# Performance work log

Hardware: AMD Instinct MI355X
Metric: run time of the kernel (lower is better)

The kernel has to match this reference:

```python
import jax, jax.numpy as jnp
import numpy as np

B, T, N = 1, 1024, 8
D_S, D_R, H, TOPK = 1024, 512, 8, 4
DH_S, DH_R = D_S // H, D_R // H
EPS = 1e-6


def _rmsnorm(x, w):
    return x * jax.lax.rsqrt(jnp.mean(x * x, axis=-1, keepdims=True) + EPS) * w


def setup_inputs() -> dict:
    key = jax.random.key(0)
    ks = jax.random.split(key, 12)

    def lin(k, fan_in, fan_out):
        b = 1.0 / np.sqrt(fan_in)
        return jax.random.uniform(k, (fan_in, fan_out), jnp.float32, -b, b)

    return {
        "s": jax.random.normal(ks[0], (B, T, D_S), jnp.float32),
        "r": jax.random.normal(ks[1], (B, T, N, D_R), jnp.float32),
        "gate_v": jax.random.uniform(ks[2], (B, T, 1), dtype=jnp.float32),
        "norm_s_w": jnp.ones((D_S,), jnp.float32),
        "norm_r_w": jnp.ones((D_R,), jnp.float32),
        "Wsq": lin(ks[3], D_S, D_S),
        "Wsk": lin(ks[4], D_R, D_S),
        "Wsv": lin(ks[5], D_R, D_S),
        "Wso": lin(ks[6], D_S, D_S),
        "Wrq": lin(ks[7], D_R, D_R),
        "Wrk": lin(ks[8], D_S, D_R),
        "Wrv": lin(ks[9], D_S, D_R),
        "Wro": lin(ks[10], D_R, D_R),
    }


def reference(s, r, gate_v, norm_s_w, norm_r_w, Wsq, Wsk, Wsv, Wso, Wrq, Wrk, Wrv, Wro):
    scale_s = DH_S ** -0.5
    scale_r = DH_R ** -0.5
    s_n = _rmsnorm(s, norm_s_w)  # (B,T,D_S)
    r_n = _rmsnorm(r, norm_r_w)  # (B,T,N,D_R)

    # --- s reads its own prefix-local reasoning slots (_s_reads_prefix_r) ---
    q = (s_n @ Wsq).reshape(B, T, H, DH_S)
    k = (r_n @ Wsk).reshape(B, T, N, H, DH_S)
    v = (r_n @ Wsv).reshape(B, T, N, H, DH_S)
    w = jax.nn.softmax(jnp.einsum('bthd,btnhd->bthn', q, k) * scale_s, axis=-1)
    s2 = s + jnp.einsum('bthn,btnhd->bthd', w, v).reshape(B, T, D_S) @ Wso

    # --- reasoning slots attend causally over surface prefix (_r_reads_s_causal) ---
    qr = (r_n @ Wrq).reshape(B, T, N, H, DH_R)
    kr = (s_n @ Wrk).reshape(B, T, H, DH_R)
    vr = (s_n @ Wrv).reshape(B, T, H, DH_R)
    scores = jnp.einsum('btnhd,bphd->btnhp', qr, kr) * scale_r  # (B,T,N,H,T)
    causal = jnp.arange(T)[:, None] >= jnp.arange(T)[None, :]  # p <= t
    scores = jnp.where(causal[None, :, None, None, :], scores, -jnp.inf)
    wr = jax.nn.softmax(scores, axis=-1)
    r2 = r + jnp.einsum('btnhp,bphd->btnhd', wr, vr).reshape(B, T, N, D_R) @ Wro

    # --- sparse top-k prefix write-back (_sparse_prefix_r_to_s) ---
    qs = s_n @ Wsq                       # (B,T,D_S)
    ksp = r_n @ Wsk                      # (B,T,N,D_S)
    vsp = r_n @ Wsv                      # (B,T,N,D_S)
    sp = jnp.einsum('btd,btnd->btn', qs, ksp) * scale_s
    vals, idx = jax.lax.top_k(sp, TOPK)
    wk = jax.nn.softmax(vals, axis=-1)   # softmax over scattered -inf == softmax over top-k
    onehot = jax.nn.one_hot(idx, N, dtype=sp.dtype)  # (B,T,K,N)
    weights = jnp.einsum('btk,btkn->btn', wk, onehot)
    r_sparse = jnp.einsum('btn,btnd->btd', weights, vsp)

    return (s2 + gate_v * r_sparse, r2)
```

## Files before the change

kernel.cpp:

```cpp
#include <hip/hip_runtime.h>
#include <hip/hip_bf16.h>
#include <math.h>
#include <type_traits>


#define T_DIM 1024
#define N_SLOT 8
#define DS 1024
#define DR 512
#define NH 8
#define DHS 128
#define DHR 64

typedef __attribute__((ext_vector_type(8))) short short8v;
typedef __attribute__((ext_vector_type(4))) float floatx4;

#define GLDS(gptr, lptr)                                                     \
  __builtin_amdgcn_global_load_lds(                                          \
      (__attribute__((address_space(1))) void*)(gptr),                       \
      (__attribute__((address_space(3))) void*)(lptr), 16, 0, 0)

__device__ inline int xcd_swz(int b, int G) {
  int per = G >> 3, rem = G & 7;
  int x = b & 7, i = b >> 3;
  return x * per + (x < rem ? x : rem) + i;
}

__device__ inline float bf_lo(unsigned int u) {
  unsigned short x = (unsigned short)(u & 0xffff);
  __hip_bfloat16 b;
  __builtin_memcpy(&b, &x, 2);
  return __bfloat162float(b);
}
__device__ inline float bf_hi(unsigned int u) {
  unsigned short x = (unsigned short)(u >> 16);
  __hip_bfloat16 b;
  __builtin_memcpy(&b, &x, 2);
  return __bfloat162float(b);
}

struct TJob { const float* W; __hip_bfloat16* Wt; int K; int N; float scale; int b0; };
struct TJobs { TJob j[8]; };

__global__ __launch_bounds__(256) void prep_kernel(
    TJobs jobs, const float* __restrict__ s, const float* __restrict__ r,
    const float* __restrict__ nsw, const float* __restrict__ nrw,
    __hip_bfloat16* __restrict__ s_nb, float* __restrict__ s_n32,
    __hip_bfloat16* __restrict__ r_nb) {
  __shared__ float sh[32][33];
  const int tid = threadIdx.x;
  if (blockIdx.x < 4608) {
    int ji = 0;
#pragma unroll
    for (int t = 1; t < 8; ++t)
      if ((int)blockIdx.x >= jobs.j[t].b0) ji = t;
    const TJob J = jobs.j[ji];
    const int lb = blockIdx.x - J.b0;
    const int nbx = J.N >> 5;
    const int n0 = (lb % nbx) * 32, k0 = (lb / nbx) * 32;
    const int tx = tid & 31, ty = tid >> 5;
#pragma unroll
    for (int i = 0; i < 4; ++i) {
      int kk = ty + i * 8;
      sh[kk][tx] = J.W[(size_t)(k0 + kk) * J.N + n0 + tx];
    }
    __syncthreads();
#pragma unroll
    for (int i = 0; i < 4; ++i) {
      int nn = ty + i * 8;
      J.Wt[(size_t)(n0 + nn) * J.K + k0 + tx] = __float2bfloat16(sh[tx][nn] * J.scale);
    }
  } else {
    const int blk = blockIdx.x - 4608;
    const bool is_s = blk < 1024;
    const int row = is_s ? blk : blk - 1024;
    const int width = is_s ? DS : DR;
    const float* x = is_s ? s : r;
    const float* w = is_s ? nsw : nrw;
    const size_t base = (size_t)row * width;
    float ss = 0.f;
    for (int i = tid; i < width; i += 256) {
      float v = x[base + i];
      ss += v * v;
    }
    for (int m = 32; m >= 1; m >>= 1) ss += __shfl_xor(ss, m);
    const int wave = tid >> 6, lane = tid & 63;
    if (lane == 0) sh[0][wave] = ss;
    __syncthreads();
    float total = sh[0][0] + sh[0][1] + sh[0][2] + sh[0][3];
    float scale = rsqrtf(total / (float)width + 1e-6f);
    for (int i = tid; i < width; i += 256) {
      float val = x[base + i] * scale * w[i];
      if (is_s) {
        s_nb[base + i] = __float2bfloat16(val);
        s_n32[base + i] = val;
      } else {
        r_nb[base + i] = __float2bfloat16(val);
      }
    }
  }
}

template <int BS, int TT, bool BT, bool BSUM>
__global__ __launch_bounds__(256) void gemm_f32_kernel(
    const float* __restrict__ A, const float* __restrict__ B,
    float* __restrict__ C, int M, int N, int K) {
  __shared__ __align__(16) float Ast[16][BS + 4];
  __shared__ __align__(16) float Bs[16][BS + 4];
  const int tid = threadIdx.x;
  const int tx = tid & 15, ty = tid >> 4;
  const int row0 = blockIdx.y * BS, col0 = blockIdx.x * BS;
  const int kz = blockIdx.z;
  const int kbeg = kz * (K >> 1), kend = kbeg + (K >> 1);
  float* Cz = C + (size_t)kz * M * N;
  const size_t bsz = (size_t)K * N;
  float acc[TT][TT] = {};
  constexpr int NF4 = BS * 16 / 4;
  for (int k0 = kbeg; k0 < kend; k0 += 16) {
    __syncthreads();
    for (int l = tid; l < NF4; l += 256) {
      int lr = l >> 2, lk = (l & 3) << 2;
      float4 a4 = *(const float4*)&A[(size_t)(row0 + lr) * K + k0 + lk];
      Ast[lk + 0][lr] = a4.x;
      Ast[lk + 1][lr] = a4.y;
      Ast[lk + 2][lr] = a4.z;
      Ast[lk + 3][lr] = a4.w;
      if (BT) {
        float4 b4 = *(const float4*)&B[(size_t)(col0 + lr) * K + k0 + lk];
        Bs[lk + 0][lr] = b4.x;
        Bs[lk + 1][lr] = b4.y;
        Bs[lk + 2][lr] = b4.z;
        Bs[lk + 3][lr] = b4.w;
      } else {
        int bkk = l / (BS / 4), bc = (l % (BS / 4)) << 2;
        size_t bidx = (size_t)(k0 + bkk) * N + col0 + bc;
        float4 b4 = *(const float4*)&B[bidx];
        if (BSUM) {
          float4 b2 = *(const float4*)&B[bsz + bidx];
          b4.x += b2.x; b4.y += b2.y; b4.z += b2.z; b4.w += b2.w;
        }
        *(float4*)&Bs[bkk][bc] = b4;
      }
    }
    __syncthreads();
#pragma unroll
    for (int kk = 0; kk < 16; ++kk) {
      float av[TT], bv[TT];
#pragma unroll
      for (int u = 0; u < TT; u += 4) {
        *(float4*)&av[u] = *(const float4*)&Ast[kk][ty * TT + u];
        *(float4*)&bv[u] = *(const float4*)&Bs[kk][tx * TT + u];
      }
#pragma unroll
      for (int i = 0; i < TT; ++i)
#pragma unroll
        for (int j = 0; j < TT; ++j) acc[i][j] += av[i] * bv[j];
    }
  }
#pragma unroll
  for (int i = 0; i < TT; ++i) {
    size_t crow = (size_t)(row0 + ty * TT + i) * N + col0;
#pragma unroll
    for (int j = 0; j < TT; j += 4) {
      *(float4*)&Cz[crow + tx * TT + j] =
          make_float4(acc[i][j], acc[i][j + 1], acc[i][j + 2], acc[i][j + 3]);
    }
  }
}

template <int MT, bool ACCUM, typename OutT, bool RADD = false>
__global__ __launch_bounds__(256) void mfma_gemm_kernel(
    const __hip_bfloat16* __restrict__ A, const __hip_bfloat16* __restrict__ Bt,
    OutT* __restrict__ C, const float* __restrict__ R, int M, int N, int K,
    int nbx) {
  constexpr int FR = MT / 32;
  constexpr int HALF = MT / 2;
  constexpr int SEG_PER_WAVE = MT / 16 / 4;
  __shared__ __hip_bfloat16 As[MT][32];
  __shared__ __hip_bfloat16 Bs[MT][32];
  const int sb = xcd_swz(blockIdx.x, gridDim.x);
  const int row0 = (sb / nbx) * MT, col0 = (sb % nbx) * MT;
  const int tid = threadIdx.x;
  const int lane = tid & 63, wave = tid >> 6;
  const int wm = wave >> 1, wn = wave & 1;
  const int l15 = lane & 15, l4 = lane >> 4;
  const int dma_r = lane >> 2;
  const int dma_c = (lane & 3) ^ ((lane >> 3) & 3);
  const int rd_sw = (l15 >> 1) & 3;
  floatx4 acc[FR][FR] = {};
  for (int k0 = 0; k0 < K; k0 += 32) {
    __syncthreads();
#pragma unroll
    for (int i = 0; i < SEG_PER_WAVE; ++i) {
      int seg = wave * SEG_PER_WAVE + i;
      GLDS(&A[(size_t)(row0 + seg * 16 + dma_r) * K + k0 + dma_c * 8], &As[seg * 16][0]);
      GLDS(&Bt[(size_t)(col0 + seg * 16 + dma_r) * K + k0 + dma_c * 8], &Bs[seg * 16][0]);
    }
    __syncthreads();
    short8v af[FR], bf[FR];
#pragma unroll
    for (int i = 0; i < FR; ++i)
      af[i] = *(const short8v*)&As[wm * HALF + i * 16 + l15][(l4 ^ rd_sw) * 8];
#pragma unroll
    for (int j = 0; j < FR; ++j)
      bf[j] = *(const short8v*)&Bs[wn * HALF + j * 16 + l15][(l4 ^ rd_sw) * 8];
#pragma unroll
    for (int i = 0; i < FR; ++i)
#pragma unroll
      for (int j = 0; j < FR; ++j)
        acc[i][j] = __builtin_amdgcn_mfma_f32_16x16x32_bf16(af[i], bf[j], acc[i][j], 0, 0, 0);
  }
#pragma unroll
  for (int i = 0; i < FR; ++i) {
    int rb = row0 + wm * HALF + i * 16 + l4 * 4;
#pragma unroll
    for (int j = 0; j < FR; ++j) {
      int cb = col0 + wn * HALF + j * 16 + l15;
#pragma unroll
      for (int rg = 0; rg < 4; ++rg) {
        size_t idx = (size_t)(rb + rg) * N + cb;
        if constexpr (std::is_same<OutT, __hip_bfloat16>::value) {
          C[idx] = __float2bfloat16(acc[i][j][rg]);
        } else if constexpr (RADD) {
          C[idx] = R[idx] + acc[i][j][rg];
        } else if constexpr (ACCUM) {
          C[idx] += acc[i][j][rg];
        } else {
          C[idx] = acc[i][j][rg];
        }
      }
    }
  }
}

struct GJob { const __hip_bfloat16* Bt; __hip_bfloat16* C; int N; int b0; int trans; };
struct GJobs { GJob j[3]; };

template <int MT>
__global__ __launch_bounds__(256) void mfma_gemm_batch_kernel(
    const __hip_bfloat16* __restrict__ A, GJobs jobs, int M, int K) {
  constexpr int FR = MT / 32;
  constexpr int HALF = MT / 2;
  constexpr int SEG_PER_WAVE = MT / 16 / 4;
  __shared__ __hip_bfloat16 As[MT][32];
  __shared__ __hip_bfloat16 Bs[MT][32];
  const int sb = xcd_swz(blockIdx.x, gridDim.x);
  int ji = 0;
#pragma unroll
  for (int t = 1; t < 3; ++t)
    if (sb >= jobs.j[t].b0) ji = t;
  const GJob J = jobs.j[ji];
  const int lb = sb - J.b0;
  const int nbx = J.N / MT;
  const int row0 = (lb / nbx) * MT, col0 = (lb % nbx) * MT;
  const int tid = threadIdx.x;
  const int lane = tid & 63, wave = tid >> 6;
  const int wm = wave >> 1, wn = wave & 1;
  const int l15 = lane & 15, l4 = lane >> 4;
  const int dma_r = lane >> 2;
  const int dma_c = (lane & 3) ^ ((lane >> 3) & 3);
  const int rd_sw = (l15 >> 1) & 3;
  floatx4 acc[FR][FR] = {};
  for (int k0 = 0; k0 < K; k0 += 32) {
    __syncthreads();
#pragma unroll
    for (int i = 0; i < SEG_PER_WAVE; ++i) {
      int seg = wave * SEG_PER_WAVE + i;
      GLDS(&A[(size_t)(row0 + seg * 16 + dma_r) * K + k0 + dma_c * 8], &As[seg * 16][0]);
      GLDS(&J.Bt[(size_t)(col0 + seg * 16 + dma_r) * K + k0 + dma_c * 8], &Bs[seg * 16][0]);
    }
    __syncthreads();
    short8v af[FR], bf[FR];
#pragma unroll
    for (int i = 0; i < FR; ++i)
      af[i] = *(const short8v*)&As[wm * HALF + i * 16 + l15][(l4 ^ rd_sw) * 8];
#pragma unroll
    for (int j = 0; j < FR; ++j)
      bf[j] = *(const short8v*)&Bs[wn * HALF + j * 16 + l15][(l4 ^ rd_sw) * 8];
#pragma unroll
    for (int i = 0; i < FR; ++i)
#pragma unroll
      for (int j = 0; j < FR; ++j)
        acc[i][j] = __builtin_amdgcn_mfma_f32_16x16x32_bf16(af[i], bf[j], acc[i][j], 0, 0, 0);
  }
#pragma unroll
  for (int i = 0; i < FR; ++i) {
    int rb = row0 + wm * HALF + i * 16 + l4 * 4;
#pragma unroll
    for (int j = 0; j < FR; ++j) {
      int cb = col0 + wn * HALF + j * 16 + l15;
      if (J.trans) {
        __hip_bfloat16 pk[4];
#pragma unroll
        for (int rg = 0; rg < 4; ++rg) pk[rg] = __float2bfloat16(acc[i][j][rg]);
        *(ushort4*)&J.C[(size_t)cb * M + rb] = *(const ushort4*)pk;
      } else {
#pragma unroll
        for (int rg = 0; rg < 4; ++rg)
          J.C[(size_t)(rb + rg) * J.N + cb] = __float2bfloat16(acc[i][j][rg]);
      }
    }
  }
}

__global__ __launch_bounds__(256) void part1_kernel(
    const float* __restrict__ s, const float* __restrict__ gv,
    const __hip_bfloat16* __restrict__ q, const __hip_bfloat16* __restrict__ k,
    const __hip_bfloat16* __restrict__ v, const float* __restrict__ r,
    const float* __restrict__ nrw, const float* __restrict__ u0,
    const float* __restrict__ u1, __hip_bfloat16* __restrict__ attn1,
    float* __restrict__ outS) {
  __shared__ float qs[DS];
  __shared__ float dots[NH][N_SLOT];
  __shared__ float wattn[NH][N_SLOT];
  __shared__ float w8[N_SLOT];
  __shared__ float spv[N_SLOT];
  __shared__ float gateL;
  const int t = blockIdx.x;
  const int tid = threadIdx.x;
  {
    const unsigned int* q2 = (const unsigned int*)&q[(size_t)t * DS];
    for (int i = tid; i < DS / 2; i += 256) {
      unsigned int pk = q2[i];
      qs[2 * i] = bf_lo(pk);
      qs[2 * i + 1] = bf_hi(pk);
    }
  }
  __syncthreads();
  const int wave = tid >> 6, lane = tid & 63;
#pragma unroll
  for (int e = 0; e < 16; ++e) {
    int pair = wave * 16 + e;
    int h = pair >> 3, n = pair & 7;
    const unsigned int* kr2 =
        (const unsigned int*)&k[((size_t)t * N_SLOT + n) * DS + h * DHS];
    unsigned int pk = kr2[lane];
    float a = qs[h * DHS + 2 * lane] * bf_lo(pk) +
              qs[h * DHS + 2 * lane + 1] * bf_hi(pk);
    for (int m = 32; m >= 1; m >>= 1) a += __shfl_xor(a, m);
    if (lane == 0) dots[h][n] = a;
  }
  const float scale_s = 0.08838834764831845f;
#pragma unroll
  for (int e = 0; e < 2; ++e) {
    const int n = wave * 2 + e;
    const float* rr = &r[((size_t)t * N_SLOT + n) * DR];
    const float* ub0 = &u0[(size_t)t * DR];
    const float* ub1 = &u1[(size_t)t * DR];
    float ssum = 0.f, dot = 0.f;
#pragma unroll
    for (int jj = 0; jj < 8; ++jj) {
      int j = lane + 64 * jj;
      float rv = rr[j];
      ssum += rv * rv;
      dot += rv * nrw[j] * (ub0[j] + ub1[j]);
    }
    for (int m = 32; m >= 1; m >>= 1) {
      ssum += __shfl_xor(ssum, m);
      dot += __shfl_xor(dot, m);
    }
    if (lane == 0) {
      float rs = rsqrtf(ssum / (float)DR + 1e-6f);
      spv[n] = scale_s * rs * dot;
    }
  }
  __syncthreads();
  if (tid < 8) {
    int h = tid;
    float vmax = -1e30f;
    for (int n = 0; n < 8; ++n) vmax = fmaxf(vmax, dots[h][n] * scale_s);
    float sum = 0.f;
    for (int n = 0; n < 8; ++n) {
      float e = __expf(dots[h][n] * scale_s - vmax);
      wattn[h][n] = e;
      sum += e;
    }
    float inv = 1.f / sum;
    for (int n = 0; n < 8; ++n) wattn[h][n] *= inv;
  }
  if (tid == 64) {
    float sv[8];
    for (int n = 0; n < 8; ++n) sv[n] = spv[n];
    bool used[8] = {};
    float vals[4];
    int idxs[4];
    for (int kk = 0; kk < 4; ++kk) {
      float best = -1e30f;
      int bi = 0;
      for (int n = 0; n < 8; ++n)
        if (!used[n] && sv[n] > best) { best = sv[n]; bi = n; }
      used[bi] = true;
      vals[kk] = best;
      idxs[kk] = bi;
    }
    float mx = vals[0];
    float wv[4];
    float sum = 0.f;
    for (int kk = 0; kk < 4; ++kk) {
      wv[kk] = __expf(vals[kk] - mx);
      sum += wv[kk];
    }
    float inv = 1.f / sum;
    for (int n = 0; n < 8; ++n) w8[n] = 0.f;
    for (int kk = 0; kk < 4; ++kk) w8[idxs[kk]] = wv[kk] * inv;
    gateL = gv[t];
  }
  __syncthreads();
  const float gate = gateL;
#pragma unroll
  for (int jj = 0; jj < 2; ++jj) {
    int dp = tid + 256 * jj;
    int hh = dp >> 6;
    float a1x = 0.f, a1y = 0.f, a2x = 0.f, a2y = 0.f;
#pragma unroll
    for (int n = 0; n < 8; ++n) {
      unsigned int pv =
          ((const unsigned int*)&v[((size_t)t * N_SLOT + n) * DS])[dp];
      float vx = bf_lo(pv), vy = bf_hi(pv);
      float wa = wattn[hh][n], wb = w8[n];
      a1x += wa * vx; a1y += wa * vy;
      a2x += wb * vx; a2y += wb * vy;
    }
    __hip_bfloat16 pk2[2] = {__float2bfloat16(a1x), __float2bfloat16(a1y)};
    ((unsigned int*)&attn1[(size_t)t * DS])[dp] = *(const unsigned int*)pk2;
    float2 sv = ((const float2*)&s[(size_t)t * DS])[dp];
    ((float2*)&outS[(size_t)t * DS])[dp] =
        make_float2(sv.x + gate * a2x, sv.y + gate * a2y);
  }
}

__global__ __launch_bounds__(256) void flash_mfma_kernel(
    const __hip_bfloat16* __restrict__ qb, const __hip_bfloat16* __restrict__ kb,
    const __hip_bfloat16* __restrict__ vbT, __hip_bfloat16* __restrict__ rat) {
  __shared__ __align__(16) __hip_bfloat16 QP[64][72];
  __shared__ __align__(16) __hip_bfloat16 Ks[64][72];
  __shared__ __align__(16) __hip_bfloat16 Vt[64][72];
  const int tid = threadIdx.x;
  const int lane = tid & 63, wave = tid >> 6;
  const int l15 = lane & 15, l4 = lane >> 4;
  const int h = blockIdx.y;
  const int qbase = blockIdx.x * 64;
  const int s = wave * 16;

  for (int g = tid; g < 512; g += 256) {
    int rr = g >> 3, c = (g & 7) * 8;
    *(ulonglong2*)&QP[rr][c] =
        *(const ulonglong2*)&qb[(size_t)(qbase + rr) * DR + h * DHR + c];
  }
  __syncthreads();
  short8v qf[2];
#pragma unroll
  for (int kk = 0; kk < 2; ++kk)
    qf[kk] = *(const short8v*)&QP[s + l15][kk * 32 + l4 * 8];

  const int myt = (qbase + s + l15) >> 3;
  const int tmin = (qbase + s) >> 3;
  const int tmax = (qbase + s + 15) >> 3;

  float m_r = -1e30f, l_r = 0.f;
  floatx4 o[4] = {};

  const int ntiles = (((qbase + 63) >> 3) >> 6) + 1;
  for (int pt = 0; pt < ntiles; ++pt) {
    const int p0 = pt << 6;
    __syncthreads();
    for (int g = tid; g < 512; g += 256) {
      int rr = g >> 3, c = (g & 7) * 8;
      *(ulonglong2*)&Ks[rr][c] =
          *(const ulonglong2*)&kb[(size_t)(p0 + rr) * DR + h * DHR + c];
      *(ulonglong2*)&Vt[rr][c] =
          *(const ulonglong2*)&vbT[(size_t)(h * DHR + rr) * T_DIM + p0 + c];
    }
    __syncthreads();
    if (p0 > tmax) continue;
    floatx4 sc[4] = {};
#pragma unroll
    for (int j = 0; j < 4; ++j)
#pragma unroll
      for (int kk = 0; kk < 2; ++kk) {
        short8v kf = *(const short8v*)&Ks[j * 16 + l15][kk * 32 + l4 * 8];
        sc[j] = __builtin_amdgcn_mfma_f32_16x16x32_bf16(kf, qf[kk], sc[j], 0, 0, 0);
      }
    if (p0 + 63 > tmin) {
#pragma unroll
      for (int j = 0; j < 4; ++j)
#pragma unroll
        for (int rg = 0; rg < 4; ++rg)
          if (p0 + j * 16 + l4 * 4 + rg > myt) sc[j][rg] = -1e30f;
    }
    float mx = m_r;
#pragma unroll
    for (int j = 0; j < 4; ++j)
#pragma unroll
      for (int rg = 0; rg < 4; ++rg) mx = fmaxf(mx, sc[j][rg]);
    mx = fmaxf(mx, __shfl_xor(mx, 16));
    mx = fmaxf(mx, __shfl_xor(mx, 32));
    float sum = 0.f;
#pragma unroll
    for (int j = 0; j < 4; ++j)
#pragma unroll
      for (int rg = 0; rg < 4; ++rg) {
        float e = __expf(sc[j][rg] - mx);
        sc[j][rg] = e;
        sum += e;
      }
    sum += __shfl_xor(sum, 16);
    sum += __shfl_xor(sum, 32);
    const float alpha = __expf(m_r - mx);
    l_r = alpha * l_r + sum;
    m_r = mx;
#pragma unroll
    for (int j = 0; j < 4; ++j) {
      __hip_bfloat16 pk[4];
#pragma unroll
      for (int rg = 0; rg < 4; ++rg) pk[rg] = __float2bfloat16(sc[j][rg]);
      *(ushort4*)&QP[s + l15][j * 16 + l4 * 4] = *(const ushort4*)pk;
    }
#pragma unroll
    for (int jd = 0; jd < 4; ++jd) o[jd] *= alpha;
#pragma unroll
    for (int kk = 0; kk < 2; ++kk) {
      short8v pf = *(const short8v*)&QP[s + l15][kk * 32 + l4 * 8];
#pragma unroll
      for (int jd = 0; jd < 4; ++jd) {
        short8v vf = *(const short8v*)&Vt[jd * 16 + l15][kk * 32 + l4 * 8];
        o[jd] = __builtin_amdgcn_mfma_f32_16x16x32_bf16(vf, pf, o[jd], 0, 0, 0);
      }
    }
  }
  const float inv = 1.f / l_r;
  const size_t rbase = (size_t)(qbase + s + l15) * DR + h * DHR;
#pragma unroll
  for (int jd = 0; jd < 4; ++jd) {
    __hip_bfloat16 pk[4];
#pragma unroll
    for (int rg = 0; rg < 4; ++rg) pk[rg] = __float2bfloat16(o[jd][rg] * inv);
    *(ushort4*)&rat[rbase + jd * 16 + l4 * 4] = *(const ushort4*)pk;
  }
}

extern "C" void kernel_launch(void* const* d_in, const int* in_sizes, int n_in,
                              void* d_out, int out_size, void* d_ws,
                              size_t ws_size, hipStream_t stream) {
  const float* s   = (const float*)d_in[0];
  const float* r   = (const float*)d_in[1];
  const float* gv  = (const float*)d_in[2];
  const float* nsw = (const float*)d_in[3];
  const float* nrw = (const float*)d_in[4];
  const float* Wsq = (const float*)d_in[5];
  const float* Wsk = (const float*)d_in[6];
  const float* Wsv = (const float*)d_in[7];
  const float* Wso = (const float*)d_in[8];
  const float* Wrq = (const float*)d_in[9];
  const float* Wrk = (const float*)d_in[10];
  const float* Wrv = (const float*)d_in[11];
  const float* Wro = (const float*)d_in[12];

  float* outS = (float*)d_out;
  float* outR = outS + 1048576;

  char* wp = (char*)d_ws;
  float* qreg = (float*)wp;           wp += 1048576 * 4;
  __hip_bfloat16* k   = (__hip_bfloat16*)wp; wp += 8388608 * 2;
  __hip_bfloat16* v   = (__hip_bfloat16*)wp; wp += 8388608 * 2;
  __hip_bfloat16* qrb = (__hip_bfloat16*)wp; wp += 4194304 * 2;
  __hip_bfloat16* krb = (__hip_bfloat16*)wp; wp += 524288 * 2;
  __hip_bfloat16* vrbT = (__hip_bfloat16*)wp; wp += 524288 * 2;
  __hip_bfloat16* s_nb = (__hip_bfloat16*)wp; wp += 1048576 * 2;
  __hip_bfloat16* r_nb = (__hip_bfloat16*)wp; wp += 4194304 * 2;
  __hip_bfloat16* WsqT = (__hip_bfloat16*)wp; wp += 1048576 * 2;
  __hip_bfloat16* WskT = (__hip_bfloat16*)wp; wp += 524288 * 2;
  __hip_bfloat16* WsvT = (__hip_bfloat16*)wp; wp += 524288 * 2;
  __hip_bfloat16* WsoT = (__hip_bfloat16*)wp; wp += 1048576 * 2;
  __hip_bfloat16* WrqT = (__hip_bfloat16*)wp; wp += 262144 * 2;
  __hip_bfloat16* WrkT = (__hip_bfloat16*)wp; wp += 524288 * 2;
  __hip_bfloat16* WrvT = (__hip_bfloat16*)wp; wp += 524288 * 2;
  __hip_bfloat16* WroT = (__hip_bfloat16*)wp; wp += 262144 * 2;

  float* s_n32 = qreg;
  __hip_bfloat16* q = (__hip_bfloat16*)qreg;
  float* Wc01 = (float*)r_nb;
  float* u0   = (float*)((char*)r_nb + 4194304);
  float* u1   = (float*)((char*)r_nb + 6291456);
  __hip_bfloat16* attn1b = s_nb;
  __hip_bfloat16* ratb   = r_nb;

  TJobs jobs = {{
      {Wsq, WsqT, 1024, 1024, 1.f, 0},
      {Wsk, WskT, 512, 1024, 1.f, 1024},
      {Wsv, WsvT, 512, 1024, 1.f, 1536},
      {Wso, WsoT, 1024, 1024, 1.f, 2048},
      {Wrq, WrqT, 512, 512, 0.125f, 3072},
      {Wrk, WrkT, 1024, 512, 1.f, 3328},
      {Wrv, WrvT, 1024, 512, 1.f, 3840},
      {Wro, WroT, 512, 512, 1.f, 4352},
  }};
  prep_kernel<<<13824, 256, 0, stream>>>(jobs, s, r, nsw, nrw, s_nb, s_n32, r_nb);

  GJobs ga = {{
      {WskT, k, 1024, 0, 0},
      {WsvT, v, 1024, 512, 0},
      {WrqT, qrb, 512, 1024, 0},
  }};
  mfma_gemm_batch_kernel<128><<<1280, 256, 0, stream>>>(r_nb, ga, 8192, 512);

  gemm_f32_kernel<64, 4, true, false><<<dim3(8, 16, 2), 256, 0, stream>>>(Wsq, Wsk, Wc01, 1024, 512, 1024);

  gemm_f32_kernel<64, 4, false, true><<<dim3(8, 16, 2), 256, 0, stream>>>(s_n32, Wc01, u0, 1024, 512, 1024);

  GJobs gb = {{
      {WsqT, q, 1024, 0, 0},
      {WrkT, krb, 512, 256, 0},
      {WrvT, vrbT, 512, 384, 1},
  }};
  mfma_gemm_batch_kernel<64><<<512, 256, 0, stream>>>(s_nb, gb, 1024, 1024);

  part1_kernel<<<1024, 256, 0, stream>>>(s, gv, q, k, v, r, nrw, u0, u1, attn1b, outS);

  mfma_gemm_kernel<64, true, float><<<256, 256, 0, stream>>>(attn1b, WsoT, outS, nullptr, 1024, 1024, 1024, 16);

  flash_mfma_kernel<<<dim3(128, 8), 256, 0, stream>>>(qrb, krb, vrbT, ratb);

  mfma_gemm_kernel<128, false, float, true><<<256, 256, 0, stream>>>(ratb, WroT, outR, r, 8192, 512, 512, 4);
}
```

Baseline: 318.9 us.

## Merge kernel launches into horizontally fused prep, GEMM, attention and epilogue kernels

Collapses the nine launches into four. The fp32 weight-combine GEMM is folded into the prep kernel. The fp32 u-GEMM and all six bf16 projection GEMMs run in one 128-tile merged kernel. The causal flash attention and the part1 per-token attention share one launch, and the two output projections share one epilogue kernel. Flash attention also gains register double-buffering of K/V tiles, and its query tiles are issued longest-first. Aliased workspace buffers are split into separate regions so the fused stages no longer overwrite each other's inputs. The aim is to cut launch gaps and tail underutilisation, at the cost of larger heterogeneous kernels whose register and shared-memory use is sized for the worst branch.

```diff
diff --git a/kernel.cpp b/kernel.cpp
--- a/kernel.cpp
+++ b/kernel.cpp
@@ -39,80 +39,18 @@
   return __bfloat162float(b);
 }
 
-struct TJob { const float* W; __hip_bfloat16* Wt; int K; int N; float scale; int b0; };
-struct TJobs { TJob j[8]; };
-
-__global__ __launch_bounds__(256) void prep_kernel(
-    TJobs jobs, const float* __restrict__ s, const float* __restrict__ r,
-    const float* __restrict__ nsw, const float* __restrict__ nrw,
-    __hip_bfloat16* __restrict__ s_nb, float* __restrict__ s_n32,
-    __hip_bfloat16* __restrict__ r_nb) {
-  __shared__ float sh[32][33];
-  const int tid = threadIdx.x;
-  if (blockIdx.x < 4608) {
-    int ji = 0;
-#pragma unroll
-    for (int t = 1; t < 8; ++t)
-      if ((int)blockIdx.x >= jobs.j[t].b0) ji = t;
-    const TJob J = jobs.j[ji];
-    const int lb = blockIdx.x - J.b0;
-    const int nbx = J.N >> 5;
-    const int n0 = (lb % nbx) * 32, k0 = (lb / nbx) * 32;
-    const int tx = tid & 31, ty = tid >> 5;
-#pragma unroll
-    for (int i = 0; i < 4; ++i) {
-      int kk = ty + i * 8;
-      sh[kk][tx] = J.W[(size_t)(k0 + kk) * J.N + n0 + tx];
-    }
-    __syncthreads();
-#pragma unroll
-    for (int i = 0; i < 4; ++i) {
-      int nn = ty + i * 8;
-      J.Wt[(size_t)(n0 + nn) * J.K + k0 + tx] = __float2bfloat16(sh[tx][nn] * J.scale);
-    }
-  } else {
-    const int blk = blockIdx.x - 4608;
-    const bool is_s = blk < 1024;
-    const int row = is_s ? blk : blk - 1024;
-    const int width = is_s ? DS : DR;
-    const float* x = is_s ? s : r;
-    const float* w = is_s ? nsw : nrw;
-    const size_t base = (size_t)row * width;
-    float ss = 0.f;
-    for (int i = tid; i < width; i += 256) {
-      float v = x[base + i];
-      ss += v * v;
-    }
-    for (int m = 32; m >= 1; m >>= 1) ss += __shfl_xor(ss, m);
-    const int wave = tid >> 6, lane = tid & 63;
-    if (lane == 0) sh[0][wave] = ss;
-    __syncthreads();
-    float total = sh[0][0] + sh[0][1] + sh[0][2] + sh[0][3];
-    float scale = rsqrtf(total / (float)width + 1e-6f);
-    for (int i = tid; i < width; i += 256) {
-      float val = x[base + i] * scale * w[i];
-      if (is_s) {
-        s_nb[base + i] = __float2bfloat16(val);
-        s_n32[base + i] = val;
-      } else {
-        r_nb[base + i] = __float2bfloat16(val);
-      }
-    }
-  }
-}
-
-template <int BS, int TT, bool BT, bool BSUM>
-__global__ __launch_bounds__(256) void gemm_f32_kernel(
-    const float* __restrict__ A, const float* __restrict__ B,
-    float* __restrict__ C, int M, int N, int K) {
-  __shared__ __align__(16) float Ast[16][BS + 4];
-  __shared__ __align__(16) float Bs[16][BS + 4];
+template <bool BT, bool BSUM>
+__device__ void gemm_f32_body(char* smemraw, const float* __restrict__ A,
+                              const float* __restrict__ B, float* __restrict__ C,
+                              int M, int N, int K, int bx, int by, int bz) {
+  constexpr int BS = 64, TT = 4;
+  float(*Ast)[BS + 4] = (float(*)[BS + 4])smemraw;
+  float(*Bs)[BS + 4] = (float(*)[BS + 4])(smemraw + 16 * (BS + 4) * 4);
   const int tid = threadIdx.x;
   const int tx = tid & 15, ty = tid >> 4;
-  const int row0 = blockIdx.y * BS, col0 = blockIdx.x * BS;
-  const int kz = blockIdx.z;
-  const int kbeg = kz * (K >> 1), kend = kbeg + (K >> 1);
-  float* Cz = C + (size_t)kz * M * N;
+  const int row0 = by * BS, col0 = bx * BS;
+  const int kbeg = bz * (K >> 1), kend = kbeg + (K >> 1);
+  float* Cz = C + (size_t)bz * M * N;
   const size_t bsz = (size_t)K * N;
   float acc[TT][TT] = {};
   constexpr int NF4 = BS * 16 / 4;
@@ -146,11 +84,8 @@
 #pragma unroll
     for (int kk = 0; kk < 16; ++kk) {
       float av[TT], bv[TT];
-#pragma unroll
-      for (int u = 0; u < TT; u += 4) {
-        *(float4*)&av[u] = *(const float4*)&Ast[kk][ty * TT + u];
-        *(float4*)&bv[u] = *(const float4*)&Bs[kk][tx * TT + u];
-      }
+      *(float4*)&av[0] = *(const float4*)&Ast[kk][ty * TT];
+      *(float4*)&bv[0] = *(const float4*)&Bs[kk][tx * TT];
 #pragma unroll
       for (int i = 0; i < TT; ++i)
 #pragma unroll
@@ -168,18 +103,104 @@
   }
 }
 
-template <int MT, bool ACCUM, typename OutT, bool RADD = false>
-__global__ __launch_bounds__(256) void mfma_gemm_kernel(
-    const __hip_bfloat16* __restrict__ A, const __hip_bfloat16* __restrict__ Bt,
-    OutT* __restrict__ C, const float* __restrict__ R, int M, int N, int K,
-    int nbx) {
-  constexpr int FR = MT / 32;
-  constexpr int HALF = MT / 2;
-  constexpr int SEG_PER_WAVE = MT / 16 / 4;
-  __shared__ __hip_bfloat16 As[MT][32];
-  __shared__ __hip_bfloat16 Bs[MT][32];
+struct TJob { const float* W; __hip_bfloat16* Wt; int K; int N; float scale; int b0; };
+struct TJobs { TJob j[8]; };
+
+__global__ __launch_bounds__(256) void prep_kernel(
+    TJobs jobs, const float* __restrict__ s, const float* __restrict__ r,
+    const float* __restrict__ nsw, const float* __restrict__ nrw,
+    __hip_bfloat16* __restrict__ s_nb, float* __restrict__ s_n32,
+    __hip_bfloat16* __restrict__ r_nb, const float* __restrict__ Wsq,
+    const float* __restrict__ Wsk, float* __restrict__ Wc01) {
+  __shared__ __align__(16) char smem[8704];
+  const int tid = threadIdx.x;
+  const int b = blockIdx.x;
+  if (b >= 13824) {
+    const int lb = b - 13824;
+    gemm_f32_body<true, false>(smem, Wsq, Wsk, Wc01, 1024, 512, 1024,
+                               lb & 7, (lb & 127) >> 3, lb >> 7);
+    return;
+  }
+  if (b < 4608) {
+    float(*t)[33] = (float(*)[33])smem;
+    int ji = 0;
+#pragma unroll
+    for (int q = 1; q < 8; ++q)
+      if (b >= jobs.j[q].b0) ji = q;
+    const TJob J = jobs.j[ji];
+    const int lb = b - J.b0;
+    const int nbx = J.N >> 5;
+    const int n0 = (lb % nbx) * 32, k0 = (lb / nbx) * 32;
+    const int tx = tid & 31, ty = tid >> 5;
+#pragma unroll
+    for (int i = 0; i < 4; ++i) {
+      int kk = ty + i * 8;
+      t[kk][tx] = J.W[(size_t)(k0 + kk) * J.N + n0 + tx];
+    }
+    __syncthreads();
+#pragma unroll
+    for (int i = 0; i < 4; ++i) {
+      int nn = ty + i * 8;
+      J.Wt[(size_t)(n0 + nn) * J.K + k0 + tx] = __float2bfloat16(t[tx][nn] * J.scale);
+    }
+  } else {
+    const int blk = b - 4608;
+    const bool is_s = blk < 1024;
+    const int row = is_s ? blk : blk - 1024;
+    const int width = is_s ? DS : DR;
+    const float* x = is_s ? s : r;
+    const float* w = is_s ? nsw : nrw;
+    const size_t base = (size_t)row * width;
+    float* red = (float*)smem;
+    float ss = 0.f;
+    for (int i = tid; i < width; i += 256) {
+      float v = x[base + i];
+      ss += v * v;
+    }
+    for (int m = 32; m >= 1; m >>= 1) ss += __shfl_xor(ss, m);
+    const int wave = tid >> 6, lane = tid & 63;
+    if (lane == 0) red[wave] = ss;
+    __syncthreads();
+    float total = red[0] + red[1] + red[2] + red[3];
+    float scale = rsqrtf(total / (float)width + 1e-6f);
+    for (int i = tid; i < width; i += 256) {
+      float val = x[base + i] * scale * w[i];
+      if (is_s) {
+        s_nb[base + i] = __float2bfloat16(val);
+        s_n32[base + i] = val;
+      } else {
+        r_nb[base + i] = __float2bfloat16(val);
+      }
+    }
+  }
+}
+
+struct GJob6 { const __hip_bfloat16* A; const __hip_bfloat16* Bt;
+               __hip_bfloat16* C; int M; int N; int K; int b0; int trans; };
+struct GJobs6 { GJob6 j[6]; };
+
+__global__ __launch_bounds__(256) void merged_gemm_kernel(
+    GJobs6 jobs, const float* __restrict__ s_n32, const float* __restrict__ Wc01,
+    float* __restrict__ u01) {
+  __shared__ __align__(16) char smem[16384];
   const int sb = xcd_swz(blockIdx.x, gridDim.x);
-  const int row0 = (sb / nbx) * MT, col0 = (sb % nbx) * MT;
+  if (sb >= 1408) {
+    const int lb = sb - 1408;
+    gemm_f32_body<false, true>(smem, s_n32, Wc01, u01, 1024, 512, 1024,
+                               lb & 7, (lb & 127) >> 3, lb >> 7);
+    return;
+  }
+  int ji = 0;
+#pragma unroll
+  for (int t = 1; t < 6; ++t)
+    if (sb >= jobs.j[t].b0) ji = t;
+  const GJob6 J = jobs.j[ji];
+  const int lb = sb - J.b0;
+  const int nbx = J.N >> 7;
+  const int row0 = (lb / nbx) * 128, col0 = (lb % nbx) * 128;
+  const int K = J.K;
+  __hip_bfloat16(*As)[32] = (__hip_bfloat16(*)[32])smem;
+  __hip_bfloat16(*Bs)[32] = (__hip_bfloat16(*)[32])(smem + 8192);
   const int tid = threadIdx.x;
   const int lane = tid & 63, wave = tid >> 6;
   const int wm = wave >> 1, wn = wave & 1;
@@ -187,72 +208,314 @@
   const int dma_r = lane >> 2;
   const int dma_c = (lane & 3) ^ ((lane >> 3) & 3);
   const int rd_sw = (l15 >> 1) & 3;
-  floatx4 acc[FR][FR] = {};
+  floatx4 acc[4][4] = {};
   for (int k0 = 0; k0 < K; k0 += 32) {
     __syncthreads();
 #pragma unroll
-    for (int i = 0; i < SEG_PER_WAVE; ++i) {
-      int seg = wave * SEG_PER_WAVE + i;
-      GLDS(&A[(size_t)(row0 + seg * 16 + dma_r) * K + k0 + dma_c * 8], &As[seg * 16][0]);
-      GLDS(&Bt[(size_t)(col0 + seg * 16 + dma_r) * K + k0 + dma_c * 8], &Bs[seg * 16][0]);
-    }
-    __syncthreads();
-    short8v af[FR], bf[FR];
-#pragma unroll
-    for (int i = 0; i < FR; ++i)
-      af[i] = *(const short8v*)&As[wm * HALF + i * 16 + l15][(l4 ^ rd_sw) * 8];
-#pragma unroll
-    for (int j = 0; j < FR; ++j)
-      bf[j] = *(const short8v*)&Bs[wn * HALF + j * 16 + l15][(l4 ^ rd_sw) * 8];
-#pragma unroll
-    for (int i = 0; i < FR; ++i)
-#pragma unroll
-      for (int j = 0; j < FR; ++j)
+    for (int i = 0; i < 2; ++i) {
+      int seg = wave * 2 + i;
+      GLDS(&J.A[(size_t)(row0 + seg * 16 + dma_r) * K + k0 + dma_c * 8], &As[seg * 16][0]);
+      GLDS(&J.Bt[(size_t)(col0 + seg * 16 + dma_r) * K + k0 + dma_c * 8], &Bs[seg * 16][0]);
+    }
+    __syncthreads();
+    short8v af[4], bf[4];
+#pragma unroll
+    for (int i = 0; i < 4; ++i)
+      af[i] = *(const short8v*)&As[wm * 64 + i * 16 + l15][(l4 ^ rd_sw) * 8];
+#pragma unroll
+    for (int j = 0; j < 4; ++j)
+      bf[j] = *(const short8v*)&Bs[wn * 64 + j * 16 + l15][(l4 ^ rd_sw) * 8];
+#pragma unroll
+    for (int i = 0; i < 4; ++i)
+#pragma unroll
+      for (int j = 0; j < 4; ++j)
         acc[i][j] = __builtin_amdgcn_mfma_f32_16x16x32_bf16(af[i], bf[j], acc[i][j], 0, 0, 0);
   }
 #pragma unroll
-  for (int i = 0; i < FR; ++i) {
-    int rb = row0 + wm * HALF + i * 16 + l4 * 4;
-#pragma unroll
-    for (int j = 0; j < FR; ++j) {
-      int cb = col0 + wn * HALF + j * 16 + l15;
-#pragma unroll
-      for (int rg = 0; rg < 4; ++rg) {
-        size_t idx = (size_t)(rb + rg) * N + cb;
-        if constexpr (std::is_same<OutT, __hip_bfloat16>::value) {
-          C[idx] = __float2bfloat16(acc[i][j][rg]);
-        } else if constexpr (RADD) {
-          C[idx] = R[idx] + acc[i][j][rg];
-        } else if constexpr (ACCUM) {
-          C[idx] += acc[i][j][rg];
-        } else {
-          C[idx] = acc[i][j][rg];
+  for (int i = 0; i < 4; ++i) {
+    int rb = row0 + wm * 64 + i * 16 + l4 * 4;
+#pragma unroll
+    for (int j = 0; j < 4; ++j) {
+      int cb = col0 + wn * 64 + j * 16 + l15;
+      if (J.trans) {
+        __hip_bfloat16 pk[4];
+#pragma unroll
+        for (int rg = 0; rg < 4; ++rg) pk[rg] = __float2bfloat16(acc[i][j][rg]);
+        *(ushort4*)&J.C[(size_t)cb * J.M + rb] = *(const ushort4*)pk;
+      } else {
+#pragma unroll
+        for (int rg = 0; rg < 4; ++rg)
+          J.C[(size_t)(rb + rg) * J.N + cb] = __float2bfloat16(acc[i][j][rg]);
+      }
+    }
+  }
+}
+
+__global__ __launch_bounds__(256) void fused_attn_kernel(
+    const __hip_bfloat16* __restrict__ qb, const __hip_bfloat16* __restrict__ kb,
+    const __hip_bfloat16* __restrict__ vbT, __hip_bfloat16* __restrict__ rat,
+    const float* __restrict__ s, const float* __restrict__ gv,
+    const __hip_bfloat16* __restrict__ q, const __hip_bfloat16* __restrict__ k,
+    const __hip_bfloat16* __restrict__ v, const float* __restrict__ r,
+    const float* __restrict__ nrw, const float* __restrict__ u0,
+    const float* __restrict__ u1, __hip_bfloat16* __restrict__ attn1,
+    float* __restrict__ outS) {
+  __shared__ __align__(16) char smem[27648];
+  const int tid = threadIdx.x;
+  if (blockIdx.x < 1024) {
+    __hip_bfloat16(*QP)[72] = (__hip_bfloat16(*)[72])smem;
+    __hip_bfloat16(*Ks)[72] = (__hip_bfloat16(*)[72])(smem + 9216);
+    __hip_bfloat16(*Vt)[72] = (__hip_bfloat16(*)[72])(smem + 18432);
+    const int fb = blockIdx.x;
+    const int qt = 127 - (fb >> 3);
+    const int h = fb & 7;
+    const int qbase = qt * 64;
+    const int lane = tid & 63, wave = tid >> 6;
+    const int l15 = lane & 15, l4 = lane >> 4;
+    const int st = wave * 16;
+
+    for (int g = tid; g < 512; g += 256) {
+      int rr = g >> 3, c = (g & 7) * 8;
+      *(ulonglong2*)&QP[rr][c] =
+          *(const ulonglong2*)&qb[(size_t)(qbase + rr) * DR + h * DHR + c];
+    }
+    __syncthreads();
+    short8v qf[2];
+#pragma unroll
+    for (int kk = 0; kk < 2; ++kk)
+      qf[kk] = *(const short8v*)&QP[st + l15][kk * 32 + l4 * 8];
+
+    const int myt = (qbase + st + l15) >> 3;
+    const int tmin = (qbase + st) >> 3;
+    const int tmax = (qbase + st + 15) >> 3;
+
+    float m_r = -1e30f, l_r = 0.f;
+    floatx4 o[4] = {};
+
+    const int rr0 = tid >> 3, c0 = (tid & 7) * 8;
+    const int g1 = tid + 256;
+    const int rr1 = g1 >> 3, c1 = (g1 & 7) * 8;
+    ulonglong2 kreg0, kreg1, vreg0, vreg1;
+    auto loadKV = [&](int p0) {
+      kreg0 = *(const ulonglong2*)&kb[(size_t)(p0 + rr0) * DR + h * DHR + c0];
+      kreg1 = *(const ulonglong2*)&kb[(size_t)(p0 + rr1) * DR + h * DHR + c1];
+      vreg0 = *(const ulonglong2*)&vbT[(size_t)(h * DHR + rr0) * T_DIM + p0 + c0];
+      vreg1 = *(const ulonglong2*)&vbT[(size_t)(h * DHR + rr1) * T_DIM + p0 + c1];
+    };
+    const int ntiles = (((qbase + 63) >> 3) >> 6) + 1;
+    loadKV(0);
+    for (int pt = 0; pt < ntiles; ++pt) {
+      const int p0 = pt << 6;
+      __syncthreads();
+      *(ulonglong2*)&Ks[rr0][c0] = kreg0;
+      *(ulonglong2*)&Ks[rr1][c1] = kreg1;
+      *(ulonglong2*)&Vt[rr0][c0] = vreg0;
+      *(ulonglong2*)&Vt[rr1][c1] = vreg1;
+      if (pt + 1 < ntiles) loadKV((pt + 1) << 6);
+      __syncthreads();
+      if (p0 > tmax) continue;
+      floatx4 sc[4] = {};
+#pragma unroll
+      for (int j = 0; j < 4; ++j)
+#pragma unroll
+        for (int kk = 0; kk < 2; ++kk) {
+          short8v kf = *(const short8v*)&Ks[j * 16 + l15][kk * 32 + l4 * 8];
+          sc[j] = __builtin_amdgcn_mfma_f32_16x16x32_bf16(kf, qf[kk], sc[j], 0, 0, 0);
         }
-      }
-    }
-  }
-}
-
-struct GJob { const __hip_bfloat16* Bt; __hip_bfloat16* C; int N; int b0; int trans; };
-struct GJobs { GJob j[3]; };
-
-template <int MT>
-__global__ __launch_bounds__(256) void mfma_gemm_batch_kernel(
-    const __hip_bfloat16* __restrict__ A, GJobs jobs, int M, int K) {
-  constexpr int FR = MT / 32;
-  constexpr int HALF = MT / 2;
-  constexpr int SEG_PER_WAVE = MT / 16 / 4;
-  __shared__ __hip_bfloat16 As[MT][32];
-  __shared__ __hip_bfloat16 Bs[MT][32];
+      if (p0 + 63 > tmin) {
+#pragma unroll
+        for (int j = 0; j < 4; ++j)
+#pragma unroll
+          for (int rg = 0; rg < 4; ++rg)
+            if (p0 + j * 16 + l4 * 4 + rg > myt) sc[j][rg] = -1e30f;
+      }
+      float mx = m_r;
+#pragma unroll
+      for (int j = 0; j < 4; ++j)
+#pragma unroll
+        for (int rg = 0; rg < 4; ++rg) mx = fmaxf(mx, sc[j][rg]);
+      mx = fmaxf(mx, __shfl_xor(mx, 16));
+      mx = fmaxf(mx, __shfl_xor(mx, 32));
+      float sum = 0.f;
+#pragma unroll
+      for (int j = 0; j < 4; ++j)
+#pragma unroll
+        for (int rg = 0; rg < 4; ++rg) {
+          float e = __expf(sc[j][rg] - mx);
+          sc[j][rg] = e;
+          sum += e;
+        }
+      sum += __shfl_xor(sum, 16);
+      sum += __shfl_xor(sum, 32);
+      const float alpha = __expf(m_r - mx);
+      l_r = alpha * l_r + sum;
+      m_r = mx;
+#pragma unroll
+      for (int j = 0; j < 4; ++j) {
+        __hip_bfloat16 pk[4];
+#pragma unroll
+        for (int rg = 0; rg < 4; ++rg) pk[rg] = __float2bfloat16(sc[j][rg]);
+        *(ushort4*)&QP[st + l15][j * 16 + l4 * 4] = *(const ushort4*)pk;
+      }
+#pragma unroll
+      for (int jd = 0; jd < 4; ++jd) o[jd] *= alpha;
+#pragma unroll
+      for (int kk = 0; kk < 2; ++kk) {
+        short8v pf = *(const short8v*)&QP[st + l15][kk * 32 + l4 * 8];
+#pragma unroll
+        for (int jd = 0; jd < 4; ++jd) {
+          short8v vf = *(const short8v*)&Vt[jd * 16 + l15][kk * 32 + l4 * 8];
+          o[jd] = __builtin_amdgcn_mfma_f32_16x16x32_bf16(vf, pf, o[jd], 0, 0, 0);
+        }
+      }
+    }
+    const float inv = 1.f / l_r;
+    const size_t rbase = (size_t)(qbase + st + l15) * DR + h * DHR;
+#pragma unroll
+    for (int jd = 0; jd < 4; ++jd) {
+      __hip_bfloat16 pk[4];
+#pragma unroll
+      for (int rg = 0; rg < 4; ++rg) pk[rg] = __float2bfloat16(o[jd][rg] * inv);
+      *(ushort4*)&rat[rbase + jd * 16 + l4 * 4] = *(const ushort4*)pk;
+    }
+  } else {
+    float* qs = (float*)smem;
+    float(*dots)[8] = (float(*)[8])(smem + 4096);
+    float(*wattn)[8] = (float(*)[8])(smem + 4352);
+    float* w8 = (float*)(smem + 4608);
+    float* spv = (float*)(smem + 4640);
+    float* gateL = (float*)(smem + 4672);
+    const int t = blockIdx.x - 1024;
+    {
+      const unsigned int* q2 = (const unsigned int*)&q[(size_t)t * DS];
+      for (int i = tid; i < DS / 2; i += 256) {
+        unsigned int pk = q2[i];
+        qs[2 * i] = bf_lo(pk);
+        qs[2 * i + 1] = bf_hi(pk);
+      }
+    }
+    __syncthreads();
+    const int wave = tid >> 6, lane = tid & 63;
+#pragma unroll
+    for (int e = 0; e < 16; ++e) {
+      int pair = wave * 16 + e;
+      int h = pair >> 3, n = pair & 7;
+      const unsigned int* kr2 =
+          (const unsigned int*)&k[((size_t)t * N_SLOT + n) * DS + h * DHS];
+      unsigned int pk = kr2[lane];
+      float a = qs[h * DHS + 2 * lane] * bf_lo(pk) +
+                qs[h * DHS + 2 * lane + 1] * bf_hi(pk);
+      for (int m = 32; m >= 1; m >>= 1) a += __shfl_xor(a, m);
+      if (lane == 0) dots[h][n] = a;
+    }
+    const float scale_s = 0.08838834764831845f;
+#pragma unroll
+    for (int e = 0; e < 2; ++e) {
+      const int n = wave * 2 + e;
+      const float* rr = &r[((size_t)t * N_SLOT + n) * DR];
+      const float* ub0 = &u0[(size_t)t * DR];
+      const float* ub1 = &u1[(size_t)t * DR];
+      float ssum = 0.f, dot = 0.f;
+#pragma unroll
+      for (int jj = 0; jj < 8; ++jj) {
+        int j = lane + 64 * jj;
+        float rv = rr[j];
+        ssum += rv * rv;
+        dot += rv * nrw[j] * (ub0[j] + ub1[j]);
+      }
+      for (int m = 32; m >= 1; m >>= 1) {
+        ssum += __shfl_xor(ssum, m);
+        dot += __shfl_xor(dot, m);
+      }
+      if (lane == 0) {
+        float rs = rsqrtf(ssum / (float)DR + 1e-6f);
+        spv[n] = scale_s * rs * dot;
+      }
+    }
+    __syncthreads();
+    if (tid < 8) {
+      int h = tid;
+      float vmax = -1e30f;
+      for (int n = 0; n < 8; ++n) vmax = fmaxf(vmax, dots[h][n] * scale_s);
+      float sum = 0.f;
+      for (int n = 0; n < 8; ++n) {
+        float e = __expf(dots[h][n] * scale_s - vmax);
+        wattn[h][n] = e;
+        sum += e;
+      }
+      float inv = 1.f / sum;
+      for (int n = 0; n < 8; ++n) wattn[h][n] *= inv;
+    }
+    if (tid == 64) {
+      float sv[8];
+      for (int n = 0; n < 8; ++n) sv[n] = spv[n];
+      bool used[8] = {};
+      float vals[4];
+      int idxs[4];
+      for (int kk = 0; kk < 4; ++kk) {
+        float best = -1e30f;
+        int bi = 0;
+        for (int n = 0; n < 8; ++n)
+          if (!used[n] && sv[n] > best) { best = sv[n]; bi = n; }
+        used[bi] = true;
+        vals[kk] = best;
+        idxs[kk] = bi;
+      }
+      float mx = vals[0];
+      float wv[4];
+      float sum = 0.f;
+      for (int kk = 0; kk < 4; ++kk) {
+        wv[kk] = __expf(vals[kk] - mx);
+        sum += wv[kk];
+      }
+      float inv = 1.f / sum;
+      for (int n = 0; n < 8; ++n) w8[n] = 0.f;
+      for (int kk = 0; kk < 4; ++kk) w8[idxs[kk]] = wv[kk] * inv;
+      *gateL = gv[t];
+    }
+    __syncthreads();
+    const float gate = *gateL;
+#pragma unroll
+    for (int jj = 0; jj < 2; ++jj) {
+      int dp = tid + 256 * jj;
+      int hh = dp >> 6;
+      float a1x = 0.f, a1y = 0.f, a2x = 0.f, a2y = 0.f;
+#pragma unroll
+      for (int n = 0; n < 8; ++n) {
+        unsigned int pv =
+            ((const unsigned int*)&v[((size_t)t * N_SLOT + n) * DS])[dp];
+        float vx = bf_lo(pv), vy = bf_hi(pv);
+        float wa = wattn[hh][n], wb = w8[n];
+        a1x += wa * vx; a1y += wa * vy;
+        a2x += wb * vx; a2y += wb * vy;
+      }
+      __hip_bfloat16 pk2[2] = {__float2bfloat16(a1x), __float2bfloat16(a1y)};
+      ((unsigned int*)&attn1[(size_t)t * DS])[dp] = *(const unsigned int*)pk2;
+      float2 sv = ((const float2*)&s[(size_t)t * DS])[dp];
+      ((float2*)&outS[(size_t)t * DS])[dp] =
+          make_float2(sv.x + gate * a2x, sv.y + gate * a2y);
+    }
+  }
+}
+
+__global__ __launch_bounds__(256) void epilogue_kernel(
+    const __hip_bfloat16* __restrict__ attn1, const __hip_bfloat16* __restrict__ WsoT,
+    float* __restrict__ outS, const __hip_bfloat16* __restrict__ ratb,
+    const __hip_bfloat16* __restrict__ WroT, float* __restrict__ outR,
+    const float* __restrict__ r) {
+  __shared__ __align__(16) char smem[16384];
+  __hip_bfloat16(*As)[32] = (__hip_bfloat16(*)[32])smem;
+  __hip_bfloat16(*Bs)[32] = (__hip_bfloat16(*)[32])(smem + 8192);
   const int sb = xcd_swz(blockIdx.x, gridDim.x);
-  int ji = 0;
-#pragma unroll
-  for (int t = 1; t < 3; ++t)
-    if (sb >= jobs.j[t].b0) ji = t;
-  const GJob J = jobs.j[ji];
-  const int lb = sb - J.b0;
-  const int nbx = J.N / MT;
-  const int row0 = (lb / nbx) * MT, col0 = (lb % nbx) * MT;
+  const bool wso = (sb < 64);
+  const __hip_bfloat16* A = wso ? attn1 : ratb;
+  const __hip_bfloat16* Bt = wso ? WsoT : WroT;
+  float* C = wso ? outS : outR;
+  const int lb = wso ? sb : sb - 64;
+  const int N = wso ? 1024 : 512;
+  const int K = wso ? 1024 : 512;
+  const int nbx = N >> 7;
+  const int row0 = (lb / nbx) * 128, col0 = (lb % nbx) * 128;
   const int tid = threadIdx.x;
   const int lane = tid & 63, wave = tid >> 6;
   const int wm = wave >> 1, wn = wave & 1;
@@ -260,282 +523,44 @@
   const int dma_r = lane >> 2;
   const int dma_c = (lane & 3) ^ ((lane >> 3) & 3);
   const int rd_sw = (l15 >> 1) & 3;
-  floatx4 acc[FR][FR] = {};
+  floatx4 acc[4][4] = {};
   for (int k0 = 0; k0 < K; k0 += 32) {
     __syncthreads();
 #pragma unroll
-    for (int i = 0; i < SEG_PER_WAVE; ++i) {
-      int seg = wave * SEG_PER_WAVE + i;
+    for (int i = 0; i < 2; ++i) {
+      int seg = wave * 2 + i;
       GLDS(&A[(size_t)(row0 + seg * 16 + dma_r) * K + k0 + dma_c * 8], &As[seg * 16][0]);
-      GLDS(&J.Bt[(size_t)(col0 + seg * 16 + dma_r) * K + k0 + dma_c * 8], &Bs[seg * 16][0]);
-    }
-    __syncthreads();
-    short8v af[FR], bf[FR];
-#pragma unroll
-    for (int i = 0; i < FR; ++i)
-      af[i] = *(const short8v*)&As[wm * HALF + i * 16 + l15][(l4 ^ rd_sw) * 8];
-#pragma unroll
-    for (int j = 0; j < FR; ++j)
-      bf[j] = *(const short8v*)&Bs[wn * HALF + j * 16 + l15][(l4 ^ rd_sw) * 8];
-#pragma unroll
-    for (int i = 0; i < FR; ++i)
-#pragma unroll
-      for (int j = 0; j < FR; ++j)
+      GLDS(&Bt[(size_t)(col0 + seg * 16 + dma_r) * K + k0 + dma_c * 8], &Bs[seg * 16][0]);
+    }
+    __syncthreads();
+    short8v af[4], bf[4];
+#pragma unroll
+    for (int i = 0; i < 4; ++i)
+      af[i] = *(const short8v*)&As[wm * 64 + i * 16 + l15][(l4 ^ rd_sw) * 8];
+#pragma unroll
+    for (int j = 0; j < 4; ++j)
+      bf[j] = *(const short8v*)&Bs[wn * 64 + j * 16 + l15][(l4 ^ rd_sw) * 8];
+#pragma unroll
+    for (int i = 0; i < 4; ++i)
+#pragma unroll
+      for (int j = 0; j < 4; ++j)
         acc[i][j] = __builtin_amdgcn_mfma_f32_16x16x32_bf16(af[i], bf[j], acc[i][j], 0, 0, 0);
   }
 #pragma unroll
-  for (int i = 0; i < FR; ++i) {
-    int rb = row0 + wm * HALF + i * 16 + l4 * 4;
-#pragma unroll
-    for (int j = 0; j < FR; ++j) {
-      int cb = col0 + wn * HALF + j * 16 + l15;
-      if (J.trans) {
-        __hip_bfloat16 pk[4];
-#pragma unroll
-        for (int rg = 0; rg < 4; ++rg) pk[rg] = __float2bfloat16(acc[i][j][rg]);
-        *(ushort4*)&J.C[(size_t)cb * M + rb] = *(const ushort4*)pk;
-      } else {
-#pragma unroll
-        for (int rg = 0; rg < 4; ++rg)
-          J.C[(size_t)(rb + rg) * J.N + cb] = __float2bfloat16(acc[i][j][rg]);
-      }
-    }
-  }
-}
-
-__global__ __launch_bounds__(256) void part1_kernel(
-    const float* __restrict__ s, const float* __restrict__ gv,
-    const __hip_bfloat16* __restrict__ q, const __hip_bfloat16* __restrict__ k,
-    const __hip_bfloat16* __restrict__ v, const float* __restrict__ r,
-    const float* __restrict__ nrw, const float* __restrict__ u0,
-    const float* __restrict__ u1, __hip_bfloat16* __restrict__ attn1,
-    float* __restrict__ outS) {
-  __shared__ float qs[DS];
-  __shared__ float dots[NH][N_SLOT];
-  __shared__ float wattn[NH][N_SLOT];
-  __shared__ float w8[N_SLOT];
-  __shared__ float spv[N_SLOT];
-  __shared__ float gateL;
-  const int t = blockIdx.x;
-  const int tid = threadIdx.x;
-  {
-    const unsigned int* q2 = (const unsigned int*)&q[(size_t)t * DS];
-    for (int i = tid; i < DS / 2; i += 256) {
-      unsigned int pk = q2[i];
-      qs[2 * i] = bf_lo(pk);
-      qs[2 * i + 1] = bf_hi(pk);
-    }
-  }
-  __syncthreads();
-  const int wave = tid >> 6, lane = tid & 63;
-#pragma unroll
-  for (int e = 0; e < 16; ++e) {
-    int pair = wave * 16 + e;
-    int h = pair >> 3, n = pair & 7;
-    const unsigned int* kr2 =
-        (const unsigned int*)&k[((size_t)t * N_SLOT + n) * DS + h * DHS];
-    unsigned int pk = kr2[lane];
-    float a = qs[h * DHS + 2 * lane] * bf_lo(pk) +
-              qs[h * DHS + 2 * lane + 1] * bf_hi(pk);
-    for (int m = 32; m >= 1; m >>= 1) a += __shfl_xor(a, m);
-    if (lane == 0) dots[h][n] = a;
-  }
-  const float scale_s = 0.08838834764831845f;
-#pragma unroll
-  for (int e = 0; e < 2; ++e) {
-    const int n = wave * 2 + e;
-    const float* rr = &r[((size_t)t * N_SLOT + n) * DR];
-    const float* ub0 = &u0[(size_t)t * DR];
-    const float* ub1 = &u1[(size_t)t * DR];
-    float ssum = 0.f, dot = 0.f;
-#pragma unroll
-    for (int jj = 0; jj < 8; ++jj) {
-      int j = lane + 64 * jj;
-      float rv = rr[j];
-      ssum += rv * rv;
-      dot += rv * nrw[j] * (ub0[j] + ub1[j]);
-    }
-    for (int m = 32; m >= 1; m >>= 1) {
-      ssum += __shfl_xor(ssum, m);
-      dot += __shfl_xor(dot, m);
-    }
-    if (lane == 0) {
-      float rs = rsqrtf(ssum / (float)DR + 1e-6f);
-      spv[n] = scale_s * rs * dot;
-    }
-  }
-  __syncthreads();
-  if (tid < 8) {
-    int h = tid;
-    float vmax = -1e30f;
-    for (int n = 0; n < 8; ++n) vmax = fmaxf(vmax, dots[h][n] * scale_s);
-    float sum = 0.f;
-    for (int n = 0; n < 8; ++n) {
-      float e = __expf(dots[h][n] * scale_s - vmax);
-      wattn[h][n] = e;
-      sum += e;
-    }
-    float inv = 1.f / sum;
-    for (int n = 0; n < 8; ++n) wattn[h][n] *= inv;
-  }
-  if (tid == 64) {
-    float sv[8];
-    for (int n = 0; n < 8; ++n) sv[n] = spv[n];
-    bool used[8] = {};
-    float vals[4];
-    int idxs[4];
-    for (int kk = 0; kk < 4; ++kk) {
-      float best = -1e30f;
-      int bi = 0;
-      for (int n = 0; n < 8; ++n)
-        if (!used[n] && sv[n] > best) { best = sv[n]; bi = n; }
-      used[bi] = true;
-      vals[kk] = best;
-      idxs[kk] = bi;
-    }
-    float mx = vals[0];
-    float wv[4];
-    float sum = 0.f;
-    for (int kk = 0; kk < 4; ++kk) {
-      wv[kk] = __expf(vals[kk] - mx);
-      sum += wv[kk];
-    }
-    float inv = 1.f / sum;
-    for (int n = 0; n < 8; ++n) w8[n] = 0.f;
-    for (int kk = 0; kk < 4; ++kk) w8[idxs[kk]] = wv[kk] * inv;
-    gateL = gv[t];
-  }
-  __syncthreads();
-  const float gate = gateL;
-#pragma unroll
-  for (int jj = 0; jj < 2; ++jj) {
-    int dp = tid + 256 * jj;
-    int hh = dp >> 6;
-    float a1x = 0.f, a1y = 0.f, a2x = 0.f, a2y = 0.f;
-#pragma unroll
-    for (int n = 0; n < 8; ++n) {
-      unsigned int pv =
-          ((const unsigned int*)&v[((size_t)t * N_SLOT + n) * DS])[dp];
-      float vx = bf_lo(pv), vy = bf_hi(pv);
-      float wa = wattn[hh][n], wb = w8[n];
-      a1x += wa * vx; a1y += wa * vy;
-      a2x += wb * vx; a2y += wb * vy;
-    }
-    __hip_bfloat16 pk2[2] = {__float2bfloat16(a1x), __float2bfloat16(a1y)};
-    ((unsigned int*)&attn1[(size_t)t * DS])[dp] = *(const unsigned int*)pk2;
-    float2 sv = ((const float2*)&s[(size_t)t * DS])[dp];
-    ((float2*)&outS[(size_t)t * DS])[dp] =
-        make_float2(sv.x + gate * a2x, sv.y + gate * a2y);
-  }
-}
-
-__global__ __launch_bounds__(256) void flash_mfma_kernel(
-    const __hip_bfloat16* __restrict__ qb, const __hip_bfloat16* __restrict__ kb,
-    const __hip_bfloat16* __restrict__ vbT, __hip_bfloat16* __restrict__ rat) {
-  __shared__ __align__(16) __hip_bfloat16 QP[64][72];
-  __shared__ __align__(16) __hip_bfloat16 Ks[64][72];
-  __shared__ __align__(16) __hip_bfloat16 Vt[64][72];
-  const int tid = threadIdx.x;
-  const int lane = tid & 63, wave = tid >> 6;
-  const int l15 = lane & 15, l4 = lane >> 4;
-  const int h = blockIdx.y;
-  const int qbase = blockIdx.x * 64;
-  const int s = wave * 16;
-
-  for (int g = tid; g < 512; g += 256) {
-    int rr = g >> 3, c = (g & 7) * 8;
-    *(ulonglong2*)&QP[rr][c] =
-        *(const ulonglong2*)&qb[(size_t)(qbase + rr) * DR + h * DHR + c];
-  }
-  __syncthreads();
-  short8v qf[2];
-#pragma unroll
-  for (int kk = 0; kk < 2; ++kk)
-    qf[kk] = *(const short8v*)&QP[s + l15][kk * 32 + l4 * 8];
-
-  const int myt = (qbase + s + l15) >> 3;
-  const int tmin = (qbase + s) >> 3;
-  const int tmax = (qbase + s + 15) >> 3;
-
-  float m_r = -1e30f, l_r = 0.f;
-  floatx4 o[4] = {};
-
-  const int ntiles = (((qbase + 63) >> 3) >> 6) + 1;
-  for (int pt = 0; pt < ntiles; ++pt) {
-    const int p0 = pt << 6;
-    __syncthreads();
-    for (int g = tid; g < 512; g += 256) {
-      int rr = g >> 3, c = (g & 7) * 8;
-      *(ulonglong2*)&Ks[rr][c] =
-          *(const ulonglong2*)&kb[(size_t)(p0 + rr) * DR + h * DHR + c];
-      *(ulonglong2*)&Vt[rr][c] =
-          *(const ulonglong2*)&vbT[(size_t)(h * DHR + rr) * T_DIM + p0 + c];
-    }
-    __syncthreads();
-    if (p0 > tmax) continue;
-    floatx4 sc[4] = {};
-#pragma unroll
-    for (int j = 0; j < 4; ++j)
-#pragma unroll
-      for (int kk = 0; kk < 2; ++kk) {
-        short8v kf = *(const short8v*)&Ks[j * 16 + l15][kk * 32 + l4 * 8];
-        sc[j] = __builtin_amdgcn_mfma_f32_16x16x32_bf16(kf, qf[kk], sc[j], 0, 0, 0);
-      }
-    if (p0 + 63 > tmin) {
-#pragma unroll
-      for (int j = 0; j < 4; ++j)
-#pragma unroll
-        for (int rg = 0; rg < 4; ++rg)
-          if (p0 + j * 16 + l4 * 4 + rg > myt) sc[j][rg] = -1e30f;
-    }
-    float mx = m_r;
-#pragma unroll
-    for (int j = 0; j < 4; ++j)
-#pragma unroll
-      for (int rg = 0; rg < 4; ++rg) mx = fmaxf(mx, sc[j][rg]);
-    mx = fmaxf(mx, __shfl_xor(mx, 16));
-    mx = fmaxf(mx, __shfl_xor(mx, 32));
-    float sum = 0.f;
-#pragma unroll
-    for (int j = 0; j < 4; ++j)
+  for (int i = 0; i < 4; ++i) {
+    int rb = row0 + wm * 64 + i * 16 + l4 * 4;
+#pragma unroll
+    for (int j = 0; j < 4; ++j) {
+      int cb = col0 + wn * 64 + j * 16 + l15;
 #pragma unroll
       for (int rg = 0; rg < 4; ++rg) {
-        float e = __expf(sc[j][rg] - mx);
-        sc[j][rg] = e;
-        sum += e;
-      }
-    sum += __shfl_xor(sum, 16);
-    sum += __shfl_xor(sum, 32);
-    const float alpha = __expf(m_r - mx);
-    l_r = alpha * l_r + sum;
-    m_r = mx;
-#pragma unroll
-    for (int j = 0; j < 4; ++j) {
-      __hip_bfloat16 pk[4];
-#pragma unroll
-      for (int rg = 0; rg < 4; ++rg) pk[rg] = __float2bfloat16(sc[j][rg]);
-      *(ushort4*)&QP[s + l15][j * 16 + l4 * 4] = *(const ushort4*)pk;
-    }
-#pragma unroll
-    for (int jd = 0; jd < 4; ++jd) o[jd] *= alpha;
-#pragma unroll
-    for (int kk = 0; kk < 2; ++kk) {
-      short8v pf = *(const short8v*)&QP[s + l15][kk * 32 + l4 * 8];
-#pragma unroll
-      for (int jd = 0; jd < 4; ++jd) {
-        short8v vf = *(const short8v*)&Vt[jd * 16 + l15][kk * 32 + l4 * 8];
-        o[jd] = __builtin_amdgcn_mfma_f32_16x16x32_bf16(vf, pf, o[jd], 0, 0, 0);
-      }
-    }
-  }
-  const float inv = 1.f / l_r;
-  const size_t rbase = (size_t)(qbase + s + l15) * DR + h * DHR;
-#pragma unroll
-  for (int jd = 0; jd < 4; ++jd) {
-    __hip_bfloat16 pk[4];
-#pragma unroll
-    for (int rg = 0; rg < 4; ++rg) pk[rg] = __float2bfloat16(o[jd][rg] * inv);
-    *(ushort4*)&rat[rbase + jd * 16 + l4 * 4] = *(const ushort4*)pk;
+        size_t idx = (size_t)(rb + rg) * N + cb;
+        if (wso)
+          C[idx] += acc[i][j][rg];
+        else
+          C[idx] = r[idx] + acc[i][j][rg];
+      }
+    }
   }
 }
 
@@ -560,14 +585,19 @@
   float* outR = outS + 1048576;
 
   char* wp = (char*)d_ws;
-  float* qreg = (float*)wp;           wp += 1048576 * 4;
-  __hip_bfloat16* k   = (__hip_bfloat16*)wp; wp += 8388608 * 2;
-  __hip_bfloat16* v   = (__hip_bfloat16*)wp; wp += 8388608 * 2;
-  __hip_bfloat16* qrb = (__hip_bfloat16*)wp; wp += 4194304 * 2;
-  __hip_bfloat16* krb = (__hip_bfloat16*)wp; wp += 524288 * 2;
+  float* s_n32 = (float*)wp;                  wp += 1048576 * 4;
+  __hip_bfloat16* k    = (__hip_bfloat16*)wp; wp += 8388608 * 2;
+  __hip_bfloat16* v    = (__hip_bfloat16*)wp; wp += 8388608 * 2;
+  __hip_bfloat16* qrb  = (__hip_bfloat16*)wp; wp += 4194304 * 2;
+  __hip_bfloat16* krb  = (__hip_bfloat16*)wp; wp += 524288 * 2;
   __hip_bfloat16* vrbT = (__hip_bfloat16*)wp; wp += 524288 * 2;
   __hip_bfloat16* s_nb = (__hip_bfloat16*)wp; wp += 1048576 * 2;
   __hip_bfloat16* r_nb = (__hip_bfloat16*)wp; wp += 4194304 * 2;
+  __hip_bfloat16* q    = (__hip_bfloat16*)wp; wp += 1048576 * 2;
+  __hip_bfloat16* attn1b = (__hip_bfloat16*)wp; wp += 1048576 * 2;
+  __hip_bfloat16* ratb = (__hip_bfloat16*)wp; wp += 4194304 * 2;
+  float* Wc01 = (float*)wp;                   wp += 1048576 * 4;
+  float* u01  = (float*)wp;                   wp += 1048576 * 4;
   __hip_bfloat16* WsqT = (__hip_bfloat16*)wp; wp += 1048576 * 2;
   __hip_bfloat16* WskT = (__hip_bfloat16*)wp; wp += 524288 * 2;
   __hip_bfloat16* WsvT = (__hip_bfloat16*)wp; wp += 524288 * 2;
@@ -577,13 +607,8 @@
   __hip_bfloat16* WrvT = (__hip_bfloat16*)wp; wp += 524288 * 2;
   __hip_bfloat16* WroT = (__hip_bfloat16*)wp; wp += 262144 * 2;
 
-  float* s_n32 = qreg;
-  __hip_bfloat16* q = (__hip_bfloat16*)qreg;
-  float* Wc01 = (float*)r_nb;
-  float* u0   = (float*)((char*)r_nb + 4194304);
-  float* u1   = (float*)((char*)r_nb + 6291456);
-  __hip_bfloat16* attn1b = s_nb;
-  __hip_bfloat16* ratb   = r_nb;
+  float* u0 = u01;
+  float* u1 = u01 + 524288;
 
   TJobs jobs = {{
       {Wsq, WsqT, 1024, 1024, 1.f, 0},
@@ -595,31 +620,21 @@
       {Wrv, WrvT, 1024, 512, 1.f, 3840},
       {Wro, WroT, 512, 512, 1.f, 4352},
   }};
-  prep_kernel<<<13824, 256, 0, stream>>>(jobs, s, r, nsw, nrw, s_nb, s_n32, r_nb);
-
-  GJobs ga = {{
-      {WskT, k, 1024, 0, 0},
-      {WsvT, v, 1024, 512, 0},
-      {WrqT, qrb, 512, 1024, 0},
+  prep_kernel<<<14080, 256, 0, stream>>>(jobs, s, r, nsw, nrw, s_nb, s_n32, r_nb,
+                                         Wsq, Wsk, Wc01);
+
+  GJobs6 g6 = {{
+      {r_nb, WskT, k, 8192, 1024, 512, 0, 0},
+      {r_nb, WsvT, v, 8192, 1024, 512, 512, 0},
+      {r_nb, WrqT, qrb, 8192, 512, 512, 1024, 0},
+      {s_nb, WsqT, q, 1024, 1024, 1024, 1280, 0},
+      {s_nb, WrkT, krb, 1024, 512, 1024, 1344, 0},
+      {s_nb, WrvT, vrbT, 1024, 512, 1024, 1376, 1},
   }};
-  mfma_gemm_batch_kernel<128><<<1280, 256, 0, stream>>>(r_nb, ga, 8192, 512);
-
-  gemm_f32_kernel<64, 4, true, false><<<dim3(8, 16, 2), 256, 0, stream>>>(Wsq, Wsk, Wc01, 1024, 512, 1024);
-
-  gemm_f32_kernel<64, 4, false, true><<<dim3(8, 16, 2), 256, 0, stream>>>(s_n32, Wc01, u0, 1024, 512, 1024);
-
-  GJobs gb = {{
-      {WsqT, q, 1024, 0, 0},
-      {WrkT, krb, 512, 256, 0},
-      {WrvT, vrbT, 512, 384, 1},
-  }};
-  mfma_gemm_batch_kernel<64><<<512, 256, 0, stream>>>(s_nb, gb, 1024, 1024);
-
-  part1_kernel<<<1024, 256, 0, stream>>>(s, gv, q, k, v, r, nrw, u0, u1, attn1b, outS);
-
-  mfma_gemm_kernel<64, true, float><<<256, 256, 0, stream>>>(attn1b, WsoT, outS, nullptr, 1024, 1024, 1024, 16);
-
-  flash_mfma_kernel<<<dim3(128, 8), 256, 0, stream>>>(qrb, krb, vrbT, ratb);
-
-  mfma_gemm_kernel<128, false, float, true><<<256, 256, 0, stream>>>(ratb, WroT, outR, r, 8192, 512, 512, 4);
-}
+  merged_gemm_kernel<<<1664, 256, 0, stream>>>(g6, s_n32, Wc01, u01);
+
+  fused_attn_kernel<<<2048, 256, 0, stream>>>(qrb, krb, vrbT, ratb, s, gv, q, k,
+                                              v, r, nrw, u0, u1, attn1b, outS);
+
+  epilogue_kernel<<<320, 256, 0, stream>>>(attn1b, WsoT, outS, ratb, WroT, outR, r);
+}
```

After: 350.8 us. 1.1x slower.
